# Performance work log

Measured on AMD Instinct MI355X. Metric: run time of the kernel, lower is better.

## Reference

```python
import jax, jax.numpy as jnp
import numpy as np

L, B, D, H, P = 4096, 4, 1024, 16, 256
HD = D // H
EPS = 1e-5


def _layer_norm(x, g, b):
    m = jnp.mean(x, axis=-1, keepdims=True)
    v = jnp.mean(jnp.square(x - m), axis=-1, keepdims=True)
    return (x - m) / jnp.sqrt(v + EPS) * g + b


def setup_inputs() -> dict:
    key = jax.random.key(0)
    ks = jax.random.split(key, 8)
    w = lambda k, shape: jax.random.normal(k, shape, jnp.float32) * 0.02
    return {
        "query": jax.random.normal(ks[0], (L, B, D), jnp.float32),
        "q_w": w(ks[1], (D, D)), "q_b": jnp.zeros((D,), jnp.float32),
        "k_w": w(ks[2], (D, D)), "k_b": jnp.zeros((D,), jnp.float32),
        "v_w": w(ks[3], (D, D)), "v_b": jnp.zeros((D,), jnp.float32),
        "e_weight": w(ks[4], (1, H, P, HD)),
        "e_out_w": w(ks[5], (D, D)), "e_out_b": jnp.zeros((D,), jnp.float32),
        "ln_g": jnp.ones((D,), jnp.float32), "ln_b": jnp.zeros((D,), jnp.float32),
        "out_w": w(ks[6], (D, D)), "out_b": jnp.zeros((D,), jnp.float32),
    }


def reference(query, q_w, q_b, k_w, k_b, v_w, v_b, e_weight,
              e_out_w, e_out_b, ln_g, ln_b, out_w, out_b):
    scaling = HD ** -0.5
    # ---- _compute_kv (kv_same=True, no padding mask) ----
    # kv: (L,B,D) -> (B,H,HD,L)
    kvh = query.reshape(L, B, H, HD).transpose(1, 2, 3, 0)
    # pkv = relu(E @ (kv * scaling)) : (B,H,P,L)
    pkv = jax.nn.relu(jnp.einsum('hpd,bhdl->bhpl', e_weight[0], kvh * scaling))
    # kv = pkv @ kv^T : (B,H,P,HD)
    kv = jnp.einsum('bhpl,bhdl->bhpd', pkv, kvh)
    # -> (P,B,D), e_out linear, residual add of e_weight, layer norm
    kv = kv.transpose(2, 0, 1, 3).reshape(P, B, D)
    kv = kv @ e_out_w.T + e_out_b
    kv = kv.reshape(P, B, H, HD) + e_weight.transpose(2, 0, 1, 3)  # broadcast (P,1,H,HD)
    kv = _layer_norm(kv.reshape(P, B, D), ln_g, ln_b)  # (P,B,D)

    # ---- standard MHA against the compressed kv ----
    q = (query @ q_w.T + q_b) * scaling            # (L,B,D)
    k = kv @ k_w.T + k_b                           # (P,B,D)
    v = kv @ v_w.T + v_b                           # (P,B,D)
    qh = q.reshape(L, B, H, HD)
    kh = k.reshape(P, B, H, HD)
    vh = v.reshape(P, B, H, HD)
    logits = jnp.einsum('lbhd,pbhd->bhlp', qh, kh)
    probs = jax.nn.softmax(logits, axis=-1)
    attn = jnp.einsum('bhlp,pbhd->lbhd', probs, vh).reshape(L, B, D)
    return attn @ out_w.T + out_b
```

## Files before the change

kernel.cpp:

```cpp
#include <hip/hip_runtime.h>
#include <hip/hip_bf16.h>
#include <cstdint>
#include <cstddef>

#define LL 4096
#define BB 4
#define DD 1024
#define HH 16
#define PP 256
#define HDD 64
#define LC 16
#define LCHUNK 256

constexpr float kScaling = 0.125f;
constexpr float kEps = 1e-5f;

typedef __attribute__((ext_vector_type(8))) short bf16x8;
typedef __attribute__((ext_vector_type(4))) short short4v;
typedef __attribute__((ext_vector_type(4))) float f32x4;

#define MFMA16(a, b, c) __builtin_amdgcn_mfma_f32_16x16x32_bf16((a), (b), (c), 0, 0, 0)

__device__ __forceinline__ unsigned short f2bf(float f) {
  unsigned int u = __builtin_bit_cast(unsigned int, f);
  u += 0x7FFFu + ((u >> 16) & 1u);
  return (unsigned short)(u >> 16);
}
__device__ __forceinline__ float bf2f(unsigned short u) {
  return __builtin_bit_cast(float, ((unsigned int)u) << 16);
}

__device__ __forceinline__ void gll16(const void* g, void* l) {
  __builtin_amdgcn_global_load_lds(
      (const __attribute__((address_space(1))) unsigned int*)g,
      (__attribute__((address_space(3))) unsigned int*)l, 16, 0, 0);
}

__global__ __launch_bounds__(256) void k_cvt_all(
    const float* __restrict__ q,
    const float* __restrict__ w0, const float* __restrict__ w1,
    const float* __restrict__ w2, const float* __restrict__ w3,
    const float* __restrict__ w4, const float* __restrict__ w5,
    unsigned short* __restrict__ dq,
    unsigned short* __restrict__ d0, unsigned short* __restrict__ d1,
    unsigned short* __restrict__ d2, unsigned short* __restrict__ d3,
    unsigned short* __restrict__ d4, unsigned short* __restrict__ d5) {
  int i = blockIdx.x * 256 + threadIdx.x;
  const float* src; unsigned short* dst; int off;
  if (i < 2097152) { src = q; dst = dq; off = i; }
  else {
    int j = i - 2097152; int w = j >> 17; off = j & 131071;
    if (w == 0) { src = w0; dst = d0; }
    else if (w == 1) { src = w1; dst = d1; }
    else if (w == 2) { src = w2; dst = d2; }
    else if (w == 3) { src = w3; dst = d3; }
    else if (w == 4) { src = w4; dst = d4; }
    else { if (off >= 32768) return; src = w5; dst = d5; }
  }
  const float4* s = (const float4*)(src + (size_t)off * 8);
  float4 a = s[0], b = s[1];
  bf16x8 o;
  o[0] = f2bf(a.x); o[1] = f2bf(a.y); o[2] = f2bf(a.z); o[3] = f2bf(a.w);
  o[4] = f2bf(b.x); o[5] = f2bf(b.y); o[6] = f2bf(b.z); o[7] = f2bf(b.w);
  *(bf16x8*)(dst + (size_t)off * 8) = o;
}

__global__ __launch_bounds__(256) void k_compress_mfma(
    const unsigned short* __restrict__ qbf, const unsigned short* __restrict__ ewbf,
    unsigned short* __restrict__ parts) {
  const int bh = blockIdx.x, lc = blockIdx.y;
  const int b = bh >> 4, h = bh & 15;
  const int tid = threadIdx.x, wv = tid >> 6, lane = tid & 63;
  const int fr = lane & 15, fg = lane >> 4;

  __shared__ __align__(16) char Xl[8192];
  __shared__ __align__(16) char Xtl[8192];
  __shared__ __align__(16) char Pl[32768];

  bf16x8 ef[4][2];
#pragma unroll
  for (int pt = 0; pt < 4; ++pt)
#pragma unroll
    for (int kc = 0; kc < 2; ++kc)
      ef[pt][kc] = *(const bf16x8*)(ewbf +
          (size_t)((h * PP + wv * 64 + pt * 16 + fr) * HDD) + kc * 32 + fg * 8);

  f32x4 acc[4][4];
#pragma unroll
  for (int i = 0; i < 4; ++i)
#pragma unroll
    for (int j = 0; j < 4; ++j) acc[i][j] = (f32x4){0.f, 0.f, 0.f, 0.f};

  const int l0 = lc * LCHUNK;
  for (int t = 0; t < 4; ++t) {
    __syncthreads();
#pragma unroll
    for (int j = 0; j < 2; ++j) {
      int u = tid + j * 256;
      int l = u >> 3, c8 = u & 7;
      bf16x8 val = *(const bf16x8*)(qbf +
          ((size_t)(l0 + t * 64 + l) * BB + b) * DD + h * HDD + c8 * 8);
      *(bf16x8*)(Xl + l * 128 + ((c8 ^ (l & 7)) << 4)) = val;
#pragma unroll
      for (int i = 0; i < 8; ++i) {
        int dd = c8 * 8 + i;
        *(short*)(Xtl + dd * 128 + ((((l >> 3) ^ (dd & 7) ^ (dd >> 3)) & 7) << 4) +
                  ((l & 7) << 1)) = val[i];
      }
    }
    __syncthreads();
#pragma unroll
    for (int lt = 0; lt < 4; ++lt) {
      int rl = lt * 16 + fr;
      bf16x8 xa0 = *(const bf16x8*)(Xl + rl * 128 + (((0 + fg) ^ (rl & 7)) << 4));
      bf16x8 xa1 = *(const bf16x8*)(Xl + rl * 128 + (((4 + fg) ^ (rl & 7)) << 4));
#pragma unroll
      for (int pt = 0; pt < 4; ++pt) {
        f32x4 s = (f32x4){0.f, 0.f, 0.f, 0.f};
        s = MFMA16(xa0, ef[pt][0], s);
        s = MFMA16(xa1, ef[pt][1], s);
        short4v pk;
#pragma unroll
        for (int r = 0; r < 4; ++r)
          pk[r] = (short)f2bf(fmaxf(s[r] * kScaling, 0.f));
        int p = wv * 64 + pt * 16 + fr;
        int lbase = lt * 16 + fg * 4;
        int slot = lbase >> 3;
        *(short4v*)(Pl + p * 128 + ((slot ^ (p & 7)) << 4) + ((lbase & 7) << 1)) = pk;
      }
    }
    asm volatile("s_waitcnt lgkmcnt(0)" ::: "memory");
    __builtin_amdgcn_sched_barrier(0);
#pragma unroll
    for (int kc = 0; kc < 2; ++kc) {
      bf16x8 pa[4], xb[4];
#pragma unroll
      for (int pt = 0; pt < 4; ++pt) {
        int p = wv * 64 + pt * 16 + fr;
        pa[pt] = *(const bf16x8*)(Pl + p * 128 + (((kc * 4 + fg) ^ (p & 7)) << 4));
      }
#pragma unroll
      for (int dt = 0; dt < 4; ++dt) {
        int dd = dt * 16 + fr;
        xb[dt] = *(const bf16x8*)(Xtl + dd * 128 +
                  ((((kc * 4 + fg) ^ (dd & 7) ^ (dd >> 3)) & 7) << 4));
      }
#pragma unroll
      for (int pt = 0; pt < 4; ++pt)
#pragma unroll
        for (int dt = 0; dt < 4; ++dt)
          acc[pt][dt] = MFMA16(pa[pt], xb[dt], acc[pt][dt]);
    }
  }
  unsigned short* op = parts + (size_t)(lc * 64 + bh) * PP * HDD;
#pragma unroll
  for (int pt = 0; pt < 4; ++pt)
#pragma unroll
    for (int dt = 0; dt < 4; ++dt)
#pragma unroll
      for (int r = 0; r < 4; ++r) {
        int p = wv * 64 + pt * 16 + fg * 4 + r;
        int dd = dt * 16 + fr;
        op[(size_t)p * HDD + dd] = f2bf(acc[pt][dt][r]);
      }
}

__global__ __launch_bounds__(256) void k_reduce(const unsigned short* __restrict__ parts,
                                                unsigned short* __restrict__ kv_raw_bf) {
  int i = blockIdx.x * 256 + threadIdx.x;
  float s = 0.f;
#pragma unroll
  for (int lcc = 0; lcc < LC; ++lcc) s += bf2f(parts[(size_t)lcc * (64 * PP * HDD) + i]);
  int d = i & 63, p = (i >> 6) & 255, bh = i >> 14;
  int b = bh >> 4, h = bh & 15;
  kv_raw_bf[(size_t)(p * BB + b) * DD + h * HDD + d] = f2bf(s);
}

template <int MODE, typename OUTT>
__device__ __forceinline__ void gemm_body(
    const unsigned short* __restrict__ A, const unsigned short* __restrict__ W,
    const float* __restrict__ bias, const float* __restrict__ ew,
    OUTT* __restrict__ C, int m0, int n0, char* Al, char* Bl) {
  const int tid = threadIdx.x;
  const int wv = tid >> 6, lane = tid & 63;
  const int fr = lane & 15, fg = lane >> 4;
  const int wr = wv >> 1, wc = wv & 1;

  f32x4 acc[4][4];
#pragma unroll
  for (int i = 0; i < 4; ++i)
#pragma unroll
    for (int j = 0; j < 4; ++j) acc[i][j] = (f32x4){0.f, 0.f, 0.f, 0.f};

  for (int k0 = 0; k0 < DD; k0 += 64) {
    __syncthreads();
#pragma unroll
    for (int j = 0; j < 4; ++j) {
      int u = tid + j * 256;
      int row = u >> 3, slot = u & 7;
      size_t gcol = (size_t)(k0 + 8 * (slot ^ (row & 7)));
      gll16(A + (size_t)(m0 + row) * DD + gcol, Al + u * 16);
      gll16(W + (size_t)(n0 + row) * DD + gcol, Bl + u * 16);
    }
    __syncthreads();
#pragma unroll
    for (int kc = 0; kc < 2; ++kc) {
      bf16x8 af[4], bfr[4];
#pragma unroll
      for (int mt = 0; mt < 4; ++mt) {
        int r = wr * 64 + mt * 16 + fr;
        af[mt] = *(const bf16x8*)(Al + r * 128 + (((kc * 4 + fg) ^ (r & 7)) << 4));
      }
#pragma unroll
      for (int nt = 0; nt < 4; ++nt) {
        int r = wc * 64 + nt * 16 + fr;
        bfr[nt] = *(const bf16x8*)(Bl + r * 128 + (((kc * 4 + fg) ^ (r & 7)) << 4));
      }
#pragma unroll
      for (int mt = 0; mt < 4; ++mt)
#pragma unroll
        for (int nt = 0; nt < 4; ++nt)
          acc[mt][nt] = MFMA16(af[mt], bfr[nt], acc[mt][nt]);
    }
  }

  float bs[4];
#pragma unroll
  for (int nt = 0; nt < 4; ++nt) bs[nt] = bias[n0 + wc * 64 + nt * 16 + fr];
#pragma unroll
  for (int mt = 0; mt < 4; ++mt)
#pragma unroll
    for (int nt = 0; nt < 4; ++nt) {
      int n = n0 + wc * 64 + nt * 16 + fr;
#pragma unroll
      for (int r = 0; r < 4; ++r) {
        int m = m0 + wr * 64 + mt * 16 + fg * 4 + r;
        float v = acc[mt][nt][r] + bs[nt];
        if (MODE == 1) v *= kScaling;
        if (MODE == 2) {
          int p = m >> 2, hh = n >> 6, d2 = n & 63;
          v += ew[(size_t)((hh << 8) + p) * HDD + d2];
        }
        if constexpr (sizeof(OUTT) == 2)
          C[(size_t)m * DD + n] = (OUTT)f2bf(v);
        else
          C[(size_t)m * DD + n] = v;
      }
    }
}

template <int MODE, typename OUTT>
__global__ __launch_bounds__(256) void k_gemm_mfma(
    const unsigned short* __restrict__ A, const unsigned short* __restrict__ W,
    const float* __restrict__ bias, const float* __restrict__ ew,
    OUTT* __restrict__ C) {
  __shared__ __align__(16) char Al[16384];
  __shared__ __align__(16) char Bl[16384];
  gemm_body<MODE, OUTT>(A, W, bias, ew, C, blockIdx.x * 128, blockIdx.y * 128, Al, Bl);
}

__global__ __launch_bounds__(256) void k_gemm_kv(
    const unsigned short* __restrict__ A,
    const unsigned short* __restrict__ Wk, const unsigned short* __restrict__ Wv,
    const float* __restrict__ kb, const float* __restrict__ vb,
    unsigned short* __restrict__ Ck, unsigned short* __restrict__ Cv) {
  __shared__ __align__(16) char Al[16384];
  __shared__ __align__(16) char Bl[16384];
  if (blockIdx.z == 0)
    gemm_body<0, unsigned short>(A, Wk, kb, nullptr, Ck,
                                 blockIdx.x * 128, blockIdx.y * 128, Al, Bl);
  else
    gemm_body<0, unsigned short>(A, Wv, vb, nullptr, Cv,
                                 blockIdx.x * 128, blockIdx.y * 128, Al, Bl);
}

template <int MODE, typename OUTT>
__global__ __launch_bounds__(512, 2) void k_gemm256(
    const unsigned short* __restrict__ A, const unsigned short* __restrict__ W,
    const float* __restrict__ bias, OUTT* __restrict__ C) {
  __shared__ __align__(16) char lds[131072];
  const int tid = threadIdx.x;
  const int wv = tid >> 6, lane = tid & 63;
  const int fr = lane & 15, fg = lane >> 4;
  const int wm = wv >> 2, wn = wv & 3;
  const int m0 = blockIdx.x * 256, n0 = blockIdx.y * 256;
  const int srow = tid >> 2, sslot = tid & 3;

  auto stageHalf = [&](const unsigned short* __restrict__ G, int g0, int colbase,
                       int dstBase) {
#pragma unroll
    for (int j = 0; j < 2; ++j) {
      int row = srow + j * 128;
      int gs = sslot ^ ((row >> 1) & 3);
      gll16(G + (size_t)(g0 + row) * DD + colbase + gs * 8,
            lds + dstBase + (tid + j * 512) * 16);
    }
  };
  auto rdA = [&](int mf, int kc, int cb) -> bf16x8 {
    int r = wm * 128 + mf * 16 + fr;
    return *(const bf16x8*)(lds + cb + kc * 16384 + r * 64 +
                            ((fg ^ ((r >> 1) & 3)) << 4));
  };
  auto rdB = [&](int nf, int kc, int cb) -> bf16x8 {
    int r = wn * 64 + nf * 16 + fr;
    return *(const bf16x8*)(lds + cb + 32768 + kc * 16384 + r * 64 +
                            ((fg ^ ((r >> 1) & 3)) << 4));
  };

  f32x4 acc[8][4];
#pragma unroll
  for (int i = 0; i < 8; ++i)
#pragma unroll
    for (int j = 0; j < 4; ++j) acc[i][j] = (f32x4){0.f, 0.f, 0.f, 0.f};
  bf16x8 a[4], b[4];

  stageHalf(A, m0, 0, 0);
  stageHalf(W, n0, 0, 32768);
  stageHalf(A, m0, 32, 16384);
  stageHalf(W, n0, 32, 32768 + 16384);
  stageHalf(A, m0, 64, 65536);
  stageHalf(W, n0, 64, 65536 + 32768);
  asm volatile("s_waitcnt vmcnt(4)" ::: "memory");
  __builtin_amdgcn_s_barrier();

  const int NT = DD / 64;
  for (int t = 0; t < NT; ++t) {
    const int cb = (t & 1) << 16;
    const int nb = cb ^ 65536;
    const int k1 = (t + 1) * 64, k2 = (t + 2) * 64;

#pragma unroll
    for (int i = 0; i < 4; ++i) a[i] = rdA(i, 0, cb);
#pragma unroll
    for (int i = 0; i < 4; ++i) b[i] = rdB(i, 0, cb);
    if (t + 1 < NT) stageHalf(A, m0, k1 + 32, nb + 16384);
    __builtin_amdgcn_s_barrier();
    asm volatile("s_waitcnt lgkmcnt(0)" ::: "memory");
    __builtin_amdgcn_sched_barrier(0);
    __builtin_amdgcn_s_setprio(1);
#pragma unroll
    for (int mf = 0; mf < 4; ++mf)
#pragma unroll
      for (int nf = 0; nf < 4; ++nf)
        acc[mf][nf] = MFMA16(a[mf], b[nf], acc[mf][nf]);
    __builtin_amdgcn_s_setprio(0);
    __builtin_amdgcn_s_barrier();

#pragma unroll
    for (int i = 0; i < 4; ++i) a[i] = rdA(4 + i, 0, cb);
    if (t + 1 < NT) stageHalf(W, n0, k1 + 32, nb + 32768 + 16384);
    __builtin_amdgcn_s_barrier();
    asm volatile("s_waitcnt lgkmcnt(0)" ::: "memory");
    __builtin_amdgcn_sched_barrier(0);
    __builtin_amdgcn_s_setprio(1);
#pragma unroll
    for (int mf = 0; mf < 4; ++mf)
#pragma unroll
      for (int nf = 0; nf < 4; ++nf)
        acc[4 + mf][nf] = MFMA16(a[mf], b[nf], acc[4 + mf][nf]);
    __builtin_amdgcn_s_setprio(0);
    __builtin_amdgcn_s_barrier();

#pragma unroll
    for (int i = 0; i < 4; ++i) a[i] = rdA(i, 1, cb);
#pragma unroll
    for (int i = 0; i < 4; ++i) b[i] = rdB(i, 1, cb);
    if (t + 2 < NT) stageHalf(A, m0, k2, cb);
    __builtin_amdgcn_s_barrier();
    asm volatile("s_waitcnt lgkmcnt(0)" ::: "memory");
    __builtin_amdgcn_sched_barrier(0);
    __builtin_amdgcn_s_setprio(1);
#pragma unroll
    for (int mf = 0; mf < 4; ++mf)
#pragma unroll
      for (int nf = 0; nf < 4; ++nf)
        acc[mf][nf] = MFMA16(a[mf], b[nf], acc[mf][nf]);
    __builtin_amdgcn_s_setprio(0);
    __builtin_amdgcn_s_barrier();

#pragma unroll
    for (int i = 0; i < 4; ++i) a[i] = rdA(4 + i, 1, cb);
    if (t + 2 < NT) stageHalf(W, n0, k2, cb + 32768);
    __builtin_amdgcn_s_barrier();
    asm volatile("s_waitcnt lgkmcnt(0)" ::: "memory");
    __builtin_amdgcn_sched_barrier(0);
    __builtin_amdgcn_s_setprio(1);
#pragma unroll
    for (int mf = 0; mf < 4; ++mf)
#pragma unroll
      for (int nf = 0; nf < 4; ++nf)
        acc[4 + mf][nf] = MFMA16(a[mf], b[nf], acc[4 + mf][nf]);
    __builtin_amdgcn_s_setprio(0);
    if (t + 2 < NT) {
      asm volatile("s_waitcnt vmcnt(4)" ::: "memory");
    } else if (t + 1 < NT) {
      asm volatile("s_waitcnt vmcnt(0)" ::: "memory");
    }
    __builtin_amdgcn_s_barrier();
  }

  float bs[4];
#pragma unroll
  for (int nf = 0; nf < 4; ++nf) bs[nf] = bias[n0 + wn * 64 + nf * 16 + fr];
#pragma unroll
  for (int mf = 0; mf < 8; ++mf)
#pragma unroll
    for (int nf = 0; nf < 4; ++nf) {
      int n = n0 + wn * 64 + nf * 16 + fr;
#pragma unroll
      for (int r = 0; r < 4; ++r) {
        int m = m0 + wm * 128 + mf * 16 + fg * 4 + r;
        float v = acc[mf][nf][r] + bs[nf];
        if (MODE == 1) v *= kScaling;
        if constexpr (sizeof(OUTT) == 2)
          C[(size_t)m * DD + n] = (OUTT)f2bf(v);
        else
          C[(size_t)m * DD + n] = v;
      }
    }
}

__global__ __launch_bounds__(256) void k_ln(const float* __restrict__ x,
                                            const float* __restrict__ g,
                                            const float* __restrict__ bb,
                                            unsigned short* __restrict__ y) {
  const int r = blockIdx.x;
  const int tid = threadIdx.x;
  const float* xr = x + (size_t)r * DD;
  float4 v = *(const float4*)(xr + tid * 4);
  float s1 = v.x + v.y + v.z + v.w;
  float s2 = v.x * v.x + v.y * v.y + v.z * v.z + v.w * v.w;
#pragma unroll
  for (int off = 32; off > 0; off >>= 1) {
    s1 += __shfl_down(s1, off);
    s2 += __shfl_down(s2, off);
  }
  __shared__ float w1[4], w2[4];
  if ((tid & 63) == 0) { w1[tid >> 6] = s1; w2[tid >> 6] = s2; }
  __syncthreads();
  float S1 = w1[0] + w1[1] + w1[2] + w1[3];
  float S2 = w2[0] + w2[1] + w2[2] + w2[3];
  float mean = S1 * (1.f / DD);
  float var = S2 * (1.f / DD) - mean * mean;
  float rstd = rsqrtf(var + kEps);
  float4 gv = *(const float4*)(g + tid * 4);
  float4 bv = *(const float4*)(bb + tid * 4);
  short4v o;
  o[0] = (short)f2bf((v.x - mean) * rstd * gv.x + bv.x);
  o[1] = (short)f2bf((v.y - mean) * rstd * gv.y + bv.y);
  o[2] = (short)f2bf((v.z - mean) * rstd * gv.z + bv.z);
  o[3] = (short)f2bf((v.w - mean) * rstd * gv.w + bv.w);
  *(short4v*)(y + (size_t)r * DD + tid * 4) = o;
}

__global__ __launch_bounds__(512, 2) void k_attn_mfma(
    const unsigned short* __restrict__ qbf, const unsigned short* __restrict__ kbf,
    const unsigned short* __restrict__ vbf, unsigned short* __restrict__ attn) {
  const int bh = blockIdx.y;
  const int b = bh >> 4, h = bh & 15;
  const int tid = threadIdx.x, wv = tid >> 6, lane = tid & 63;
  const int fr = lane & 15, fg = lane >> 4;
  const int bl0 = blockIdx.x * 256;

  __shared__ __align__(16) char Kl[16384];
  __shared__ __align__(16) char Vt[16384];
  __shared__ __align__(16) char Pl[32768];

  bf16x8 qf[2][2];
#pragma unroll
  for (int ql = 0; ql < 2; ++ql) {
    const size_t qrow = ((size_t)(bl0 + ql * 128 + wv * 16 + fr) * BB + b) * DD + h * HDD;
    qf[ql][0] = *(const bf16x8*)(qbf + qrow + fg * 8);
    qf[ql][1] = *(const bf16x8*)(qbf + qrow + 32 + fg * 8);
  }

  f32x4 o[2][4];
#pragma unroll
  for (int ql = 0; ql < 2; ++ql)
#pragma unroll
    for (int dt = 0; dt < 4; ++dt) o[ql][dt] = (f32x4){0.f, 0.f, 0.f, 0.f};
  float psum[2] = {0.f, 0.f};
  char* Pw = Pl + wv * 4096;

  for (int ph = 0; ph < 2; ++ph) {
    __syncthreads();
#pragma unroll
    for (int j = 0; j < 2; ++j) {
      int u = tid + j * 512;
      int p = u >> 3, slot = u & 7;
      gll16(kbf + ((size_t)((ph * 128 + p) * BB + b)) * DD + h * HDD +
                8 * (slot ^ (p & 7)),
            Kl + u * 16);
    }
#pragma unroll
    for (int j = 0; j < 2; ++j) {
      int u = tid + j * 512;
      int p = u >> 3, c8 = u & 7;
      bf16x8 val = *(const bf16x8*)(vbf +
          ((size_t)((ph * 128 + p) * BB + b)) * DD + h * HDD + c8 * 8);
      int pc = p >> 6, pl = p & 63;
#pragma unroll
      for (int i = 0; i < 8; ++i) {
        int dd = c8 * 8 + i;
        *(short*)(Vt + pc * 8192 + dd * 128 +
                  ((((pl >> 3) ^ (dd & 7) ^ (dd >> 3)) & 7) << 4) +
                  ((pl & 7) << 1)) = val[i];
      }
    }
    __syncthreads();

#pragma unroll
    for (int ql = 0; ql < 2; ++ql) {
      f32x4 s[8];
      __builtin_amdgcn_s_setprio(1);
#pragma unroll
      for (int pt = 0; pt < 8; ++pt) {
        int pr = pt * 16 + fr;
        bf16x8 a0 = *(const bf16x8*)(Kl + pr * 128 + ((fg ^ (pr & 7)) << 4));
        bf16x8 a1 = *(const bf16x8*)(Kl + pr * 128 + (((4 + fg) ^ (pr & 7)) << 4));
        f32x4 acc = (f32x4){0.f, 0.f, 0.f, 0.f};
        acc = MFMA16(a0, qf[ql][0], acc);
        acc = MFMA16(a1, qf[ql][1], acc);
        s[pt] = acc;
      }
      __builtin_amdgcn_s_setprio(0);

      asm volatile("s_waitcnt lgkmcnt(0)" ::: "memory");
      __builtin_amdgcn_sched_barrier(0);
#pragma unroll
      for (int pt = 0; pt < 8; ++pt) {
        float e0 = __expf(s[pt][0]), e1 = __expf(s[pt][1]);
        float e2 = __expf(s[pt][2]), e3 = __expf(s[pt][3]);
        psum[ql] += (e0 + e1) + (e2 + e3);
        short4v pk;
        pk[0] = (short)f2bf(e0); pk[1] = (short)f2bf(e1);
        pk[2] = (short)f2bf(e2); pk[3] = (short)f2bf(e3);
        int pbyte = (pt * 16 + fg * 4) * 2;
        int slot = pbyte >> 4, rem = pbyte & 15;
        *(short4v*)(Pw + fr * 256 + ((slot ^ (fr & 7)) << 4) + rem) = pk;
      }
      asm volatile("s_waitcnt lgkmcnt(0)" ::: "memory");
      __builtin_amdgcn_sched_barrier(0);

      __builtin_amdgcn_s_setprio(1);
#pragma unroll
      for (int kc = 0; kc < 4; ++kc) {
        int slot = kc * 4 + fg;
        bf16x8 pa = *(const bf16x8*)(Pw + fr * 256 + ((slot ^ (fr & 7)) << 4));
        int sl2 = (kc & 1) * 4 + fg;
#pragma unroll
        for (int dt = 0; dt < 4; ++dt) {
          int dd = dt * 16 + fr;
          bf16x8 vb = *(const bf16x8*)(Vt + (kc >> 1) * 8192 + dd * 128 +
                       (((sl2 ^ (dd & 7) ^ (dd >> 3)) & 7) << 4));
          o[ql][dt] = MFMA16(pa, vb, o[ql][dt]);
        }
      }
      __builtin_amdgcn_s_setprio(0);
    }
  }

#pragma unroll
  for (int ql = 0; ql < 2; ++ql) {
    float ps = psum[ql];
    ps += __shfl_xor(ps, 16);
    ps += __shfl_xor(ps, 32);
#pragma unroll
    for (int r = 0; r < 4; ++r) {
      int lloc = fg * 4 + r;
      float inv = 1.f / __shfl(ps, lloc);
      unsigned short* op = attn +
          ((size_t)(bl0 + ql * 128 + wv * 16 + lloc) * BB + b) * DD + h * HDD;
#pragma unroll
      for (int dt = 0; dt < 4; ++dt)
        op[dt * 16 + fr] = f2bf(o[ql][dt][r] * inv);
    }
  }
}

extern "C" void kernel_launch(void* const* d_in, const int* in_sizes, int n_in,
                              void* d_out, int out_size, void* d_ws, size_t ws_size,
                              hipStream_t stream) {
  const float* query   = (const float*)d_in[0];
  const float* q_w     = (const float*)d_in[1];
  const float* q_b     = (const float*)d_in[2];
  const float* k_w     = (const float*)d_in[3];
  const float* k_b     = (const float*)d_in[4];
  const float* v_w     = (const float*)d_in[5];
  const float* v_b     = (const float*)d_in[6];
  const float* e_weight= (const float*)d_in[7];
  const float* e_out_w = (const float*)d_in[8];
  const float* e_out_b = (const float*)d_in[9];
  const float* ln_g    = (const float*)d_in[10];
  const float* ln_b    = (const float*)d_in[11];
  const float* out_w   = (const float*)d_in[12];
  const float* out_b   = (const float*)d_in[13];
  float* out = (float*)d_out;

  char* w = (char*)d_ws;
  unsigned short* parts   = (unsigned short*)w;
  unsigned short* q_bf    = (unsigned short*)w;
  unsigned short* attn_bf = (unsigned short*)(w + (32u << 20));
  unsigned short* query_bf= (unsigned short*)(w + (64u << 20));
  unsigned short* kv_raw  = (unsigned short*)(w + (96u << 20));
  float* kv_eo            = (float*)(w + (98u << 20));
  unsigned short* kv_ln   = (unsigned short*)(w + (102u << 20));
  unsigned short* k_buf   = (unsigned short*)(w + (104u << 20));
  unsigned short* v_buf   = (unsigned short*)(w + (106u << 20));
  unsigned short* wq  = (unsigned short*)(w + (108u << 20));
  unsigned short* wk  = (unsigned short*)(w + (110u << 20));
  unsigned short* wv_ = (unsigned short*)(w + (112u << 20));
  unsigned short* weo = (unsigned short*)(w + (114u << 20));
  unsigned short* wo  = (unsigned short*)(w + (116u << 20));
  unsigned short* ewb = (unsigned short*)(w + (118u << 20));

  k_cvt_all<<<10880, 256, 0, stream>>>(query, q_w, k_w, v_w, e_out_w, out_w, e_weight,
                                       query_bf, wq, wk, wv_, weo, wo, ewb);

  k_compress_mfma<<<dim3(64, LC), 256, 0, stream>>>(query_bf, ewb, parts);
  k_reduce<<<4096, 256, 0, stream>>>(parts, kv_raw);
  k_gemm_mfma<2, float><<<dim3(8, 8), 256, 0, stream>>>(kv_raw, weo, e_out_b, e_weight, kv_eo);
  k_ln<<<PP * BB, 256, 0, stream>>>(kv_eo, ln_g, ln_b, kv_ln);
  k_gemm256<1, unsigned short><<<dim3(64, 4), 512, 0, stream>>>(query_bf, wq, q_b, q_bf);
  k_gemm_kv<<<dim3(8, 8, 2), 256, 0, stream>>>(kv_ln, wk, wv_, k_b, v_b, k_buf, v_buf);
  k_attn_mfma<<<dim3(16, 64), 512, 0, stream>>>(q_bf, k_buf, v_buf, attn_bf);
  k_gemm256<0, float><<<dim3(64, 4), 512, 0, stream>>>(attn_bf, wo, out_b, out);
}
```

Measured before the change: 222.3 us.

## Halve attention rows per block and pack transposed LDS stores as pairs

The attention kernel now processes 128 query rows per block instead of 256 and launches twice as many blocks. This raises parallelism and cuts per-thread registers, at the cost of staging K/V into LDS twice as often. In both the compress and attention kernels, the transposed LDS writes now load two adjacent rows per thread and store 32-bit packed pairs instead of 16-bit scalars, halving the LDS store count. One explicit s_waitcnt before the exp stage is dropped, relying on compiler dependency tracking.

```diff
diff --git a/kernel.cpp b/kernel.cpp
--- a/kernel.cpp
+++ b/kernel.cpp
@@ -94,18 +94,22 @@
   const int l0 = lc * LCHUNK;
   for (int t = 0; t < 4; ++t) {
     __syncthreads();
-#pragma unroll
-    for (int j = 0; j < 2; ++j) {
-      int u = tid + j * 256;
-      int l = u >> 3, c8 = u & 7;
-      bf16x8 val = *(const bf16x8*)(qbf +
-          ((size_t)(l0 + t * 64 + l) * BB + b) * DD + h * HDD + c8 * 8);
-      *(bf16x8*)(Xl + l * 128 + ((c8 ^ (l & 7)) << 4)) = val;
+    {
+      int l2 = tid >> 3, c8 = tid & 7;
+      int l = 2 * l2;
+      const unsigned short* xp = qbf +
+          ((size_t)(l0 + t * 64 + l) * BB + b) * DD + h * HDD + c8 * 8;
+      bf16x8 v0 = *(const bf16x8*)xp;
+      bf16x8 v1 = *(const bf16x8*)(xp + BB * DD);
+      *(bf16x8*)(Xl + l * 128 + ((c8 ^ (l & 7)) << 4)) = v0;
+      *(bf16x8*)(Xl + (l + 1) * 128 + ((c8 ^ ((l + 1) & 7)) << 4)) = v1;
 #pragma unroll
       for (int i = 0; i < 8; ++i) {
         int dd = c8 * 8 + i;
-        *(short*)(Xtl + dd * 128 + ((((l >> 3) ^ (dd & 7) ^ (dd >> 3)) & 7) << 4) +
-                  ((l & 7) << 1)) = val[i];
+        unsigned int packed = (unsigned int)(unsigned short)v0[i] |
+                              ((unsigned int)(unsigned short)v1[i] << 16);
+        *(unsigned int*)(Xtl + dd * 128 +
+            ((((l >> 3) ^ (dd & 7) ^ (dd >> 3)) & 7) << 4) + ((l & 7) << 1)) = packed;
       }
     }
     __syncthreads();
@@ -460,26 +464,20 @@
   const int b = bh >> 4, h = bh & 15;
   const int tid = threadIdx.x, wv = tid >> 6, lane = tid & 63;
   const int fr = lane & 15, fg = lane >> 4;
-  const int bl0 = blockIdx.x * 256;
+  const int bl0 = blockIdx.x * 128;
 
   __shared__ __align__(16) char Kl[16384];
   __shared__ __align__(16) char Vt[16384];
   __shared__ __align__(16) char Pl[32768];
 
-  bf16x8 qf[2][2];
-#pragma unroll
-  for (int ql = 0; ql < 2; ++ql) {
-    const size_t qrow = ((size_t)(bl0 + ql * 128 + wv * 16 + fr) * BB + b) * DD + h * HDD;
-    qf[ql][0] = *(const bf16x8*)(qbf + qrow + fg * 8);
-    qf[ql][1] = *(const bf16x8*)(qbf + qrow + 32 + fg * 8);
-  }
-
-  f32x4 o[2][4];
-#pragma unroll
-  for (int ql = 0; ql < 2; ++ql)
-#pragma unroll
-    for (int dt = 0; dt < 4; ++dt) o[ql][dt] = (f32x4){0.f, 0.f, 0.f, 0.f};
-  float psum[2] = {0.f, 0.f};
+  const size_t qrow = ((size_t)(bl0 + wv * 16 + fr) * BB + b) * DD + h * HDD;
+  bf16x8 qf0 = *(const bf16x8*)(qbf + qrow + fg * 8);
+  bf16x8 qf1 = *(const bf16x8*)(qbf + qrow + 32 + fg * 8);
+
+  f32x4 o[4];
+#pragma unroll
+  for (int dt = 0; dt < 4; ++dt) o[dt] = (f32x4){0.f, 0.f, 0.f, 0.f};
+  float psum = 0.f;
   char* Pw = Pl + wv * 4096;
 
   for (int ph = 0; ph < 2; ++ph) {
@@ -492,89 +490,83 @@
                 8 * (slot ^ (p & 7)),
             Kl + u * 16);
     }
-#pragma unroll
-    for (int j = 0; j < 2; ++j) {
-      int u = tid + j * 512;
-      int p = u >> 3, c8 = u & 7;
-      bf16x8 val = *(const bf16x8*)(vbf +
-          ((size_t)((ph * 128 + p) * BB + b)) * DD + h * HDD + c8 * 8);
-      int pc = p >> 6, pl = p & 63;
+    {
+      int p2 = tid >> 3, c8 = tid & 7;
+      int p0 = ph * 128 + 2 * p2;
+      const unsigned short* vp = vbf + ((size_t)(p0 * BB + b)) * DD + h * HDD + c8 * 8;
+      bf16x8 v0 = *(const bf16x8*)vp;
+      bf16x8 v1 = *(const bf16x8*)(vp + BB * DD);
+      int pl = (2 * p2) & 63, pc = p2 >> 5;
+      char* base = Vt + pc * 8192;
 #pragma unroll
       for (int i = 0; i < 8; ++i) {
         int dd = c8 * 8 + i;
-        *(short*)(Vt + pc * 8192 + dd * 128 +
-                  ((((pl >> 3) ^ (dd & 7) ^ (dd >> 3)) & 7) << 4) +
-                  ((pl & 7) << 1)) = val[i];
+        unsigned int packed = (unsigned int)(unsigned short)v0[i] |
+                              ((unsigned int)(unsigned short)v1[i] << 16);
+        *(unsigned int*)(base + dd * 128 +
+            ((((pl >> 3) ^ (dd & 7) ^ (dd >> 3)) & 7) << 4) + ((pl & 7) << 1)) = packed;
       }
     }
     __syncthreads();
 
-#pragma unroll
-    for (int ql = 0; ql < 2; ++ql) {
-      f32x4 s[8];
-      __builtin_amdgcn_s_setprio(1);
-#pragma unroll
-      for (int pt = 0; pt < 8; ++pt) {
-        int pr = pt * 16 + fr;
-        bf16x8 a0 = *(const bf16x8*)(Kl + pr * 128 + ((fg ^ (pr & 7)) << 4));
-        bf16x8 a1 = *(const bf16x8*)(Kl + pr * 128 + (((4 + fg) ^ (pr & 7)) << 4));
-        f32x4 acc = (f32x4){0.f, 0.f, 0.f, 0.f};
-        acc = MFMA16(a0, qf[ql][0], acc);
-        acc = MFMA16(a1, qf[ql][1], acc);
-        s[pt] = acc;
-      }
-      __builtin_amdgcn_s_setprio(0);
-
-      asm volatile("s_waitcnt lgkmcnt(0)" ::: "memory");
-      __builtin_amdgcn_sched_barrier(0);
-#pragma unroll
-      for (int pt = 0; pt < 8; ++pt) {
-        float e0 = __expf(s[pt][0]), e1 = __expf(s[pt][1]);
-        float e2 = __expf(s[pt][2]), e3 = __expf(s[pt][3]);
-        psum[ql] += (e0 + e1) + (e2 + e3);
-        short4v pk;
-        pk[0] = (short)f2bf(e0); pk[1] = (short)f2bf(e1);
-        pk[2] = (short)f2bf(e2); pk[3] = (short)f2bf(e3);
-        int pbyte = (pt * 16 + fg * 4) * 2;
-        int slot = pbyte >> 4, rem = pbyte & 15;
-        *(short4v*)(Pw + fr * 256 + ((slot ^ (fr & 7)) << 4) + rem) = pk;
-      }
-      asm volatile("s_waitcnt lgkmcnt(0)" ::: "memory");
-      __builtin_amdgcn_sched_barrier(0);
-
-      __builtin_amdgcn_s_setprio(1);
-#pragma unroll
-      for (int kc = 0; kc < 4; ++kc) {
-        int slot = kc * 4 + fg;
-        bf16x8 pa = *(const bf16x8*)(Pw + fr * 256 + ((slot ^ (fr & 7)) << 4));
-        int sl2 = (kc & 1) * 4 + fg;
-#pragma unroll
-        for (int dt = 0; dt < 4; ++dt) {
-          int dd = dt * 16 + fr;
-          bf16x8 vb = *(const bf16x8*)(Vt + (kc >> 1) * 8192 + dd * 128 +
-                       (((sl2 ^ (dd & 7) ^ (dd >> 3)) & 7) << 4));
-          o[ql][dt] = MFMA16(pa, vb, o[ql][dt]);
-        }
-      }
-      __builtin_amdgcn_s_setprio(0);
-    }
+    f32x4 s[8];
+    __builtin_amdgcn_s_setprio(1);
+#pragma unroll
+    for (int pt = 0; pt < 8; ++pt) {
+      int pr = pt * 16 + fr;
+      bf16x8 a0 = *(const bf16x8*)(Kl + pr * 128 + ((fg ^ (pr & 7)) << 4));
+      bf16x8 a1 = *(const bf16x8*)(Kl + pr * 128 + (((4 + fg) ^ (pr & 7)) << 4));
+      f32x4 acc = (f32x4){0.f, 0.f, 0.f, 0.f};
+      acc = MFMA16(a0, qf0, acc);
+      acc = MFMA16(a1, qf1, acc);
+      s[pt] = acc;
+    }
+    __builtin_amdgcn_s_setprio(0);
+
+#pragma unroll
+    for (int pt = 0; pt < 8; ++pt) {
+      float e0 = __expf(s[pt][0]), e1 = __expf(s[pt][1]);
+      float e2 = __expf(s[pt][2]), e3 = __expf(s[pt][3]);
+      psum += (e0 + e1) + (e2 + e3);
+      short4v pk;
+      pk[0] = (short)f2bf(e0); pk[1] = (short)f2bf(e1);
+      pk[2] = (short)f2bf(e2); pk[3] = (short)f2bf(e3);
+      int pbyte = (pt * 16 + fg * 4) * 2;
+      int slot = pbyte >> 4, rem = pbyte & 15;
+      *(short4v*)(Pw + fr * 256 + ((slot ^ (fr & 7)) << 4) + rem) = pk;
+    }
+    asm volatile("s_waitcnt lgkmcnt(0)" ::: "memory");
+    __builtin_amdgcn_sched_barrier(0);
+
+    __builtin_amdgcn_s_setprio(1);
+#pragma unroll
+    for (int kc = 0; kc < 4; ++kc) {
+      int slot = kc * 4 + fg;
+      bf16x8 pa = *(const bf16x8*)(Pw + fr * 256 + ((slot ^ (fr & 7)) << 4));
+      int sl2 = (kc & 1) * 4 + fg;
+#pragma unroll
+      for (int dt = 0; dt < 4; ++dt) {
+        int dd = dt * 16 + fr;
+        bf16x8 vb = *(const bf16x8*)(Vt + (kc >> 1) * 8192 + dd * 128 +
+                     (((sl2 ^ (dd & 7) ^ (dd >> 3)) & 7) << 4));
+        o[dt] = MFMA16(pa, vb, o[dt]);
+      }
+    }
+    __builtin_amdgcn_s_setprio(0);
   }
 
-#pragma unroll
-  for (int ql = 0; ql < 2; ++ql) {
-    float ps = psum[ql];
-    ps += __shfl_xor(ps, 16);
-    ps += __shfl_xor(ps, 32);
-#pragma unroll
-    for (int r = 0; r < 4; ++r) {
-      int lloc = fg * 4 + r;
-      float inv = 1.f / __shfl(ps, lloc);
-      unsigned short* op = attn +
-          ((size_t)(bl0 + ql * 128 + wv * 16 + lloc) * BB + b) * DD + h * HDD;
-#pragma unroll
-      for (int dt = 0; dt < 4; ++dt)
-        op[dt * 16 + fr] = f2bf(o[ql][dt][r] * inv);
-    }
+  psum += __shfl_xor(psum, 16);
+  psum += __shfl_xor(psum, 32);
+
+#pragma unroll
+  for (int r = 0; r < 4; ++r) {
+    int lloc = fg * 4 + r;
+    float inv = 1.f / __shfl(psum, lloc);
+    unsigned short* op = attn +
+        ((size_t)(bl0 + wv * 16 + lloc) * BB + b) * DD + h * HDD;
+#pragma unroll
+    for (int dt = 0; dt < 4; ++dt)
+      op[dt * 16 + fr] = f2bf(o[dt][r] * inv);
   }
 }
 
@@ -623,6 +615,6 @@
   k_ln<<<PP * BB, 256, 0, stream>>>(kv_eo, ln_g, ln_b, kv_ln);
   k_gemm256<1, unsigned short><<<dim3(64, 4), 512, 0, stream>>>(query_bf, wq, q_b, q_bf);
   k_gemm_kv<<<dim3(8, 8, 2), 256, 0, stream>>>(kv_ln, wk, wv_, k_b, v_b, k_buf, v_buf);
-  k_attn_mfma<<<dim3(16, 64), 512, 0, stream>>>(q_bf, k_buf, v_buf, attn_bf);
+  k_attn_mfma<<<dim3(32, 64), 512, 0, stream>>>(q_bf, k_buf, v_buf, attn_bf);
   k_gemm256<0, float><<<dim3(64, 4), 512, 0, stream>>>(attn_bf, wo, out_b, out);
 }
```

After: 213.2 us. -4.1%, faster.
